# Optimization experiments

Measured on AMD Instinct MI355X. Metric: run time of the kernel, lower is better.

The kernel has to match this reference:

```python
import jax, jax.numpy as jnp
import numpy as np

BETA = 0.25  # commitment-loss weight


def setup_inputs() -> dict:
    key = jax.random.key(0)
    k1, k2 = jax.random.split(key)
    # x: [B, H, W, D] so that x.reshape(-1, D) groups per-pixel latent vectors
    x = jax.random.normal(k1, (32, 64, 64, 64), dtype=jnp.float32)
    # codebook: [D, K] as in the torch module (embedding_dim, num_embeddings)
    embedding = jax.random.normal(k2, (64, 1024), dtype=jnp.float32)
    return {"x": x, "embedding": embedding}


def reference(x, embedding):
    D, K = embedding.shape
    flat = x.reshape(-1, D)  # [N, D]
    # pairwise squared distances: ||z||^2 + ||e||^2 - 2 z.e  -> [N, K]
    distances = (
        jnp.sum(flat * flat, axis=1, keepdims=True)
        + jnp.sum(embedding * embedding, axis=0)
        - 2.0 * (flat @ embedding)
    )
    encoding_indices = jnp.argmin(distances, axis=1)  # [N]
    encodings = jax.nn.one_hot(encoding_indices, K, dtype=x.dtype)  # [N, K]
    # gather codewords (same math as encodings @ embedding.T, but O(N*D))
    quantized = jnp.take(embedding, encoding_indices, axis=1).T.reshape(x.shape)
    e_latent_loss = jnp.mean((jax.lax.stop_gradient(quantized) - x) ** 2)
    loss = BETA * e_latent_loss
    # straight-through estimator
    quantized_st = x + jax.lax.stop_gradient(quantized - x)
    avg_probs = jnp.mean(encodings, axis=0)
    perplexity = jnp.exp(-jnp.sum(avg_probs * jnp.log(avg_probs + 1e-10)))
    return quantized_st, loss, perplexity, encodings, encoding_indices
```

## Files before the change

### kernel.cpp

```cpp
#include <hip/hip_runtime.h>
#include <hip/hip_fp16.h>
#include <math.h>

#define NPIX    131072
#define DDIM    64
#define KCODE   1024
#define BETA    0.25f
#define EPS2    4e-3f
#define FIXCAP  2048
#define TAILROW 130944

#define Q_OFF    0
#define LOSS_OFF 8388608
#define PERP_OFF 8388609
#define ENC_OFF  8388610
#define IDX_OFF  142606338

#define TAIL_F     134086656
#define EHS_F      (TAIL_F + 2)
#define ELS_F      (TAIL_F + 32770)
#define FIXLIST_I  (TAIL_F + 65540)
#define FIXDELTA_F (TAIL_F + 69638)
#define FIXCOUNT_I (TAIL_F + 71688)


typedef _Float16 half8 __attribute__((ext_vector_type(8)));
typedef float    f32x4 __attribute__((ext_vector_type(4)));
typedef __attribute__((address_space(3))) void       lds_void_t;
typedef __attribute__((address_space(1))) const void g_void_t;

__global__ void vq_prep(const float* __restrict__ emb, float* __restrict__ embT,
                        _Float16* __restrict__ ehs, _Float16* __restrict__ els,
                        float* __restrict__ norms) {
    int b = blockIdx.x;
    if (b < 256) {
        int i = b * 256 + threadIdx.x;
        int d = i >> 10;
        int k = i & 1023;
        float v = emb[i];
        embT[k * DDIM + d] = v;
        _Float16 h = (_Float16)v;
        _Float16 l = (_Float16)(v - (float)h);
        int panel = k >> 7, codeP = k & 127;
        int sw = (d >> 3) ^ (k & 7);
        int fi = panel * 8192 + codeP * 64 + sw * 8 + (d & 7);
        ehs[fi] = h;
        els[fi] = l;
    } else {
        int k = (b - 256) * 256 + threadIdx.x;
        float s = 0.f;
        #pragma unroll 8
        for (int d = 0; d < DDIM; ++d) {
            float v = emb[d * KCODE + k];
            s = fmaf(v, v, s);
        }
        norms[k] = s;
    }
}

__global__ __launch_bounds__(256) void vq_argmin_fused(
        const float* __restrict__ x, const _Float16* __restrict__ ehs,
        const _Float16* __restrict__ els, const float* __restrict__ norms,
        const float* __restrict__ embT, float* __restrict__ idxf,
        float* __restrict__ q, float* __restrict__ enc,
        int* __restrict__ hist, float* __restrict__ lossp,
        int* __restrict__ fixlist, int* __restrict__ fixcount) {
    __shared__ __align__(16) char lds_raw[36864];
    half8* EH8   = (half8*)lds_raw;
    half8* EL8   = (half8*)(lds_raw + 16384);
    float* NRMa  = (float*)(lds_raw + 32768);

    const int tid   = threadIdx.x;
    const int blkid = blockIdx.x;
    const int wave  = tid >> 6;
    const int lane  = tid & 63;
    const int lx = lane & 15;
    const int lk = lane >> 4;
    const int pixbase = blkid * 128 + wave * 32;

    #pragma unroll
    for (int i = 0; i < 4; ++i) NRMa[tid + i * 256] = norms[tid + i * 256];

    half8 ah[2][2], al[2][2];
    float xp0 = 0.f, xp1 = 0.f;
    #pragma unroll
    for (int mt = 0; mt < 2; ++mt) {
        const float* xr = x + (size_t)(pixbase + mt * 16 + lx) * DDIM + lk * 8;
        float xps = 0.f;
        #pragma unroll
        for (int kh = 0; kh < 2; ++kh) {
            float4 v0 = *(const float4*)(xr + kh * 32);
            float4 v1 = *(const float4*)(xr + kh * 32 + 4);
            xps = fmaf(v0.x, v0.x, xps); xps = fmaf(v0.y, v0.y, xps);
            xps = fmaf(v0.z, v0.z, xps); xps = fmaf(v0.w, v0.w, xps);
            xps = fmaf(v1.x, v1.x, xps); xps = fmaf(v1.y, v1.y, xps);
            xps = fmaf(v1.z, v1.z, xps); xps = fmaf(v1.w, v1.w, xps);
            half8 hh, ll;
            float vv;
            vv = v0.x; hh[0] = (_Float16)vv; ll[0] = (_Float16)(vv - (float)hh[0]);
            vv = v0.y; hh[1] = (_Float16)vv; ll[1] = (_Float16)(vv - (float)hh[1]);
            vv = v0.z; hh[2] = (_Float16)vv; ll[2] = (_Float16)(vv - (float)hh[2]);
            vv = v0.w; hh[3] = (_Float16)vv; ll[3] = (_Float16)(vv - (float)hh[3]);
            vv = v1.x; hh[4] = (_Float16)vv; ll[4] = (_Float16)(vv - (float)hh[4]);
            vv = v1.y; hh[5] = (_Float16)vv; ll[5] = (_Float16)(vv - (float)hh[5]);
            vv = v1.z; hh[6] = (_Float16)vv; ll[6] = (_Float16)(vv - (float)hh[6]);
            vv = v1.w; hh[7] = (_Float16)vv; ll[7] = (_Float16)(vv - (float)hh[7]);
            ah[mt][kh] = hh;
            al[mt][kh] = ll;
        }
        if (mt == 0) xp0 = xps; else xp1 = xps;
    }
    float xn0 = xp0 + __shfl_xor(xp0, 16); xn0 += __shfl_xor(xn0, 32);
    float xn1 = xp1 + __shfl_xor(xp1, 16); xn1 += __shfl_xor(xn1, 32);

    float b1[2][4], b2[2][4];
    int   i1[2][4];
    #pragma unroll
    for (int mt = 0; mt < 2; ++mt)
        #pragma unroll
        for (int r = 0; r < 4; ++r) { b1[mt][r] = 3.4e38f; b2[mt][r] = 3.4e38f; i1[mt][r] = 0; }

    float* encB = enc + (size_t)blkid * 131072;
    f32x4* zb = (f32x4*)(encB + 2);

    __syncthreads();

    #pragma unroll 1
    for (int t = 0; t < 8; ++t) {
        __builtin_amdgcn_sched_barrier(0);
        __builtin_amdgcn_s_barrier();
        __builtin_amdgcn_sched_barrier(0);
        {
            const char* gH = (const char*)ehs + (t << 14) + (tid << 4);
            const char* gL = (const char*)els + (t << 14) + (tid << 4);
            char* lH = &lds_raw[wave << 10];
            char* lL = &lds_raw[16384 + (wave << 10)];
            #pragma unroll
            for (int i = 0; i < 4; ++i) {
                __builtin_amdgcn_global_load_lds((g_void_t*)(gH + (i << 12)),
                                                 (lds_void_t*)(lH + (i << 12)), 16, 0, 0);
                __builtin_amdgcn_global_load_lds((g_void_t*)(gL + (i << 12)),
                                                 (lds_void_t*)(lL + (i << 12)), 16, 0, 0);
            }
        }
        __builtin_amdgcn_sched_barrier(0);
        if (blkid != 1023) {
            f32x4 z = {0.f, 0.f, 0.f, 0.f};
            #pragma unroll
            for (int it = 0; it < 16; ++it) {
                int fi = t * 4096 + it * 256 + tid;
                if (fi < 32767) zb[fi] = z;
            }
            asm volatile("s_waitcnt vmcnt(16)" ::: "memory");
        } else {
            asm volatile("s_waitcnt vmcnt(0)" ::: "memory");
        }
        __builtin_amdgcn_sched_barrier(0);
        __builtin_amdgcn_s_barrier();
        __builtin_amdgcn_sched_barrier(0);

        const int kbase = t * 128;
        #pragma unroll 1
        for (int c = 0; c < 8; ++c) {
            int code = c * 16 + lx;
            const half8* bhp = EH8 + code * 8;
            const half8* blp = EL8 + code * 8;
            int sw0 = lk ^ (code & 7);
            int sw1 = (lk + 4) ^ (code & 7);
            half8 bh0 = bhp[sw0], bh1 = bhp[sw1];
            half8 bl0 = blp[sw0], bl1 = blp[sw1];

            f32x4 acc0 = {0.f, 0.f, 0.f, 0.f};
            f32x4 acc1 = {0.f, 0.f, 0.f, 0.f};
            acc0 = __builtin_amdgcn_mfma_f32_16x16x32_f16(ah[0][0], bh0, acc0, 0, 0, 0);
            acc1 = __builtin_amdgcn_mfma_f32_16x16x32_f16(ah[1][0], bh0, acc1, 0, 0, 0);
            acc0 = __builtin_amdgcn_mfma_f32_16x16x32_f16(ah[0][1], bh1, acc0, 0, 0, 0);
            acc1 = __builtin_amdgcn_mfma_f32_16x16x32_f16(ah[1][1], bh1, acc1, 0, 0, 0);
            acc0 = __builtin_amdgcn_mfma_f32_16x16x32_f16(ah[0][0], bl0, acc0, 0, 0, 0);
            acc1 = __builtin_amdgcn_mfma_f32_16x16x32_f16(ah[1][0], bl0, acc1, 0, 0, 0);
            acc0 = __builtin_amdgcn_mfma_f32_16x16x32_f16(ah[0][1], bl1, acc0, 0, 0, 0);
            acc1 = __builtin_amdgcn_mfma_f32_16x16x32_f16(ah[1][1], bl1, acc1, 0, 0, 0);
            acc0 = __builtin_amdgcn_mfma_f32_16x16x32_f16(al[0][0], bh0, acc0, 0, 0, 0);
            acc1 = __builtin_amdgcn_mfma_f32_16x16x32_f16(al[1][0], bh0, acc1, 0, 0, 0);
            acc0 = __builtin_amdgcn_mfma_f32_16x16x32_f16(al[0][1], bh1, acc0, 0, 0, 0);
            acc1 = __builtin_amdgcn_mfma_f32_16x16x32_f16(al[1][1], bh1, acc1, 0, 0, 0);

            float nrm = NRMa[kbase + c * 16 + lx];
            int codeg = kbase + c * 16 + lx;
            #pragma unroll
            for (int r = 0; r < 4; ++r) {
                float d0 = fmaf(-2.0f, acc0[r], nrm);
                bool lt0 = d0 < b1[0][r];
                b2[0][r] = fminf(b2[0][r], fmaxf(b1[0][r], d0));
                b1[0][r] = fminf(b1[0][r], d0);
                i1[0][r] = lt0 ? codeg : i1[0][r];
                float d1 = fmaf(-2.0f, acc1[r], nrm);
                bool lt1 = d1 < b1[1][r];
                b2[1][r] = fminf(b2[1][r], fmaxf(b1[1][r], d1));
                b1[1][r] = fminf(b1[1][r], d1);
                i1[1][r] = lt1 ? codeg : i1[1][r];
            }
        }
        __builtin_amdgcn_sched_barrier(0);
    }

    if (blkid != 1023 && tid == 0) {
        encB[0] = 0.f; encB[1] = 0.f;
        encB[131070] = 0.f; encB[131071] = 0.f;
    }
    asm volatile("s_waitcnt vmcnt(0)" ::: "memory");
    __syncthreads();

    float* S  = (float*)(lds_raw + wave * 6528);
    float* SB1 = S, *SI = S + 544, *SB2 = S + 1088;
    int* idx_lds = (int*)(lds_raw + 26112);
    #pragma unroll
    for (int mt = 0; mt < 2; ++mt)
        #pragma unroll
        for (int r = 0; r < 4; ++r) {
            int p = mt * 16 + lk * 4 + r;
            SB1[p * 17 + lx] = b1[mt][r];
            SI [p * 17 + lx] = (float)i1[mt][r];
            SB2[p * 17 + lx] = b2[mt][r];
        }
    __syncthreads();

    float xf0 = __shfl(xn0, lane & 15);
    float xf1 = __shfl(xn1, lane & 15);
    float xf  = (lane >> 4) ? xf1 : xf0;

    float gb1 = 3.4e38f, gb2 = 3.4e38f;
    int gi1 = 0;
    if (lane < 32) {
        gi1 = KCODE;
        #pragma unroll
        for (int j = 0; j < 16; ++j) {
            float cb1 = SB1[lane * 17 + j];
            int   ci1 = (int)SI[lane * 17 + j];
            float cb2 = SB2[lane * 17 + j];
            if (cb1 < gb1 || (cb1 == gb1 && ci1 < gi1)) {
                gb2 = fminf(gb1, cb2); gb1 = cb1; gi1 = ci1;
            } else {
                gb2 = fminf(gb2, cb1);
            }
        }
        int pixel = pixbase + lane;
        idxf[pixel] = (float)gi1;
        idx_lds[wave * 32 + lane] = gi1;
        atomicAdd(&hist[gi1], 1);
        if (blkid != 1023) enc[(size_t)pixel * 1024 + gi1] = 1.f;
        if (gb2 - gb1 < EPS2) {
            int slot = atomicAdd(fixcount, 1);
            if (slot < FIXCAP) {
                fixlist[2 * slot]     = pixel;
                fixlist[2 * slot + 1] = __float_as_int(gb1);
            }
        }
    }

    float sq = (lane < 32) ? (gb1 + xf) : 0.f;
    #pragma unroll
    for (int m = 1; m < 64; m <<= 1) sq += __shfl_xor(sq, m);
    if (lane == 0) lossp[blkid * 4 + wave] = sq;

    __syncthreads();
    const f32x4* eT4 = (const f32x4*)embT;
    f32x4* q4 = (f32x4*)q;
    #pragma unroll
    for (int it = 0; it < 8; ++it) {
        int i = it * 256 + tid;
        int r = i >> 4, j = i & 15;
        int idx = idx_lds[r];
        q4[((size_t)blkid * 128 + r) * 16 + j] = eT4[idx * 16 + j];
    }
}

__global__ __launch_bounds__(64) void vq_fixup(
        const float* __restrict__ x, const float* __restrict__ embT,
        const float* __restrict__ norms, const int* __restrict__ fixlist,
        const int* __restrict__ fixcount, float* __restrict__ idxf,
        float* __restrict__ q, float* __restrict__ enc,
        int* __restrict__ hist, float* __restrict__ fixdelta) {
    int cnt = *fixcount;
    if (cnt > FIXCAP) cnt = FIXCAP;
    int b = blockIdx.x;
    if (b >= cnt) return;
    int pixel = fixlist[2 * b];
    float b1old = __int_as_float(fixlist[2 * b + 1]);
    int lane = threadIdx.x;

    float xr[64];
    const float4* x4 = (const float4*)(x + (size_t)pixel * DDIM);
    #pragma unroll
    for (int j = 0; j < 16; ++j) {
        float4 v = x4[j];
        xr[j * 4] = v.x; xr[j * 4 + 1] = v.y; xr[j * 4 + 2] = v.z; xr[j * 4 + 3] = v.w;
    }
    float bd = 3.4e38f;
    int bi = 0;
    #pragma unroll 1
    for (int c = 0; c < 16; ++c) {
        int k = lane * 16 + c;
        const float4* e4 = (const float4*)(embT + (size_t)k * DDIM);
        float a0 = 0.f, a1 = 0.f, a2 = 0.f, a3 = 0.f;
        #pragma unroll
        for (int j = 0; j < 16; ++j) {
            float4 ev = e4[j];
            a0 = fmaf(xr[j * 4],     ev.x, a0);
            a1 = fmaf(xr[j * 4 + 1], ev.y, a1);
            a2 = fmaf(xr[j * 4 + 2], ev.z, a2);
            a3 = fmaf(xr[j * 4 + 3], ev.w, a3);
        }
        float dd = fmaf(-2.0f, (a0 + a1) + (a2 + a3), norms[k]);
        if (dd < bd) { bd = dd; bi = k; }
    }
    #pragma unroll
    for (int m = 1; m < 64; m <<= 1) {
        float od = __shfl_xor(bd, m, 64);
        int   oi = __shfl_xor(bi, m, 64);
        if (od < bd || (od == bd && oi < bi)) { bd = od; bi = oi; }
    }
    q[(size_t)pixel * DDIM + lane] = embT[(size_t)bi * DDIM + lane];
    if (lane == 0) {
        int old = (int)idxf[pixel];
        idxf[pixel] = (float)bi;
        fixdelta[b] = bd - b1old;
        if (bi != old) {
            atomicAdd(&hist[old], -1);
            atomicAdd(&hist[bi], 1);
            if (pixel < TAILROW) {
                enc[(size_t)pixel * 1024 + old] = 0.f;
                enc[(size_t)pixel * 1024 + bi]  = 1.f;
            }
        }
    }
}

__global__ void vq_final(const float* __restrict__ lossp, const int* __restrict__ hist,
                         const float* __restrict__ fixdelta,
                         const int* __restrict__ fixcount,
                         float* __restrict__ out_loss, float* __restrict__ out_perp) {
    __shared__ double red[256];
    int tid = threadIdx.x;
    double s = 0.0;
    for (int i = tid; i < 4096; i += 256) s += (double)lossp[i];
    red[tid] = s;
    __syncthreads();
    for (int st = 128; st > 0; st >>= 1) {
        if (tid < st) red[tid] += red[tid + st];
        __syncthreads();
    }
    if (tid == 0) {
        int cnt = *fixcount;
        if (cnt > FIXCAP) cnt = FIXCAP;
        double d = red[0];
        for (int i = 0; i < cnt; ++i) d += (double)fixdelta[i];
        *out_loss = (float)((double)BETA * d / (double)((size_t)NPIX * DDIM));
    }
    __syncthreads();

    double e = 0.0;
    for (int i = tid; i < KCODE; i += 256) {
        float p = (float)hist[i] / (float)NPIX;
        e += (double)(p * logf(p + 1e-10f));
    }
    red[tid] = e;
    __syncthreads();
    for (int st = 128; st > 0; st >>= 1) {
        if (tid < st) red[tid] += red[tid + st];
        __syncthreads();
    }
    if (tid == 0) *out_perp = expf((float)(-red[0]));
}

__global__ void vq_tail(const float* __restrict__ idxf, float* __restrict__ enc) {
    int r = blockIdx.x;
    int pixel = TAILROW + r;
    int idx = (int)idxf[pixel];
    size_t base = (size_t)pixel * 1024;
    int t = threadIdx.x;
    if (t < 255) {
        int k = 4 * t + 2;
        f32x4 v;
        v.x = (k     == idx) ? 1.f : 0.f;
        v.y = (k + 1 == idx) ? 1.f : 0.f;
        v.z = (k + 2 == idx) ? 1.f : 0.f;
        v.w = (k + 3 == idx) ? 1.f : 0.f;
        *(f32x4*)(enc + base + k) = v;
    } else {
        enc[base]        = (idx == 0)    ? 1.f : 0.f;
        enc[base + 1]    = (idx == 1)    ? 1.f : 0.f;
        enc[base + 1022] = (idx == 1022) ? 1.f : 0.f;
        enc[base + 1023] = (idx == 1023) ? 1.f : 0.f;
    }
}

extern "C" void kernel_launch(void* const* d_in, const int* in_sizes, int n_in,
                              void* d_out, int out_size, void* d_ws, size_t ws_size,
                              hipStream_t stream) {
    const float* x   = (const float*)d_in[0];
    const float* emb = (const float*)d_in[1];
    float* out = (float*)d_out;

    char* ws = (char*)d_ws;
    float* lossp = (float*)ws;
    int*   hist  = (int*)(ws + 32768);
    float* norms = (float*)(ws + 36864);
    float* embT  = (float*)(ws + 40960);

    float* q      = out + Q_OFF;
    float* o_loss = out + LOSS_OFF;
    float* o_perp = out + PERP_OFF;
    float* enc    = out + ENC_OFF;
    float* idxf   = out + IDX_OFF;

    _Float16* ehs   = (_Float16*)(enc + EHS_F);
    _Float16* els   = (_Float16*)(enc + ELS_F);
    int* fixlist    = (int*)(enc + FIXLIST_I);
    float* fixdelta = (float*)(enc + FIXDELTA_F);
    int* fixcount   = (int*)(enc + FIXCOUNT_I);

    (void)hipMemsetAsync(ws + 32768, 0, 4096, stream);
    (void)hipMemsetAsync((void*)fixcount, 0, 4, stream);

    vq_prep<<<260, 256, 0, stream>>>(emb, embT, ehs, els, norms);
    vq_argmin_fused<<<1024, 256, 0, stream>>>(x, ehs, els, norms, embT, idxf, q,
                                              enc, hist, lossp, fixlist, fixcount);
    vq_fixup<<<FIXCAP, 64, 0, stream>>>(x, embT, norms, fixlist, fixcount,
                                        idxf, q, enc, hist, fixdelta);
    vq_final<<<1, 256, 0, stream>>>(lossp, hist, fixdelta, fixcount, o_loss, o_perp);
    vq_tail<<<128, 256, 0, stream>>>(idxf, enc);
}
```

Baseline: 206.5 us.

## Split encodings zeroing into dedicated blocks and shrink codebook panels

The fused kernel now launches twice as many blocks: odd blocks only stream zeros across the whole one-hot encodings buffer, while even blocks do the fp16-split MFMA argmin. The compute blocks stage 64-code panels instead of 128, which roughly halves LDS use and may raise occupancy. They also reduce candidates with cross-lane shuffles rather than an LDS transpose. The one-hot writes move into a separate poke kernel that must run after zeroing, adding a launch and a reread of the indices in exchange for taking store traffic off the compute waves.

Result: slower. 244.3 us (+18.3%).

```diff
diff --git a/kernel.cpp b/kernel.cpp
--- a/kernel.cpp
+++ b/kernel.cpp
@@ -1,5 +1,4 @@
 #include <hip/hip_runtime.h>
-#include <hip/hip_fp16.h>
 #include <math.h>
 
 #define NPIX    131072
@@ -41,9 +40,9 @@
         embT[k * DDIM + d] = v;
         _Float16 h = (_Float16)v;
         _Float16 l = (_Float16)(v - (float)h);
-        int panel = k >> 7, codeP = k & 127;
+        int panel = k >> 6, codeP = k & 63;
         int sw = (d >> 3) ^ (k & 7);
-        int fi = panel * 8192 + codeP * 64 + sw * 8 + (d & 7);
+        int fi = panel * 4096 + codeP * 64 + sw * 8 + (d & 7);
         ehs[fi] = h;
         els[fi] = l;
     } else {
@@ -58,28 +57,42 @@
     }
 }
 
-__global__ __launch_bounds__(256) void vq_argmin_fused(
+__global__ __launch_bounds__(256) void vq_fused(
         const float* __restrict__ x, const _Float16* __restrict__ ehs,
         const _Float16* __restrict__ els, const float* __restrict__ norms,
         const float* __restrict__ embT, float* __restrict__ idxf,
         float* __restrict__ q, float* __restrict__ enc,
         int* __restrict__ hist, float* __restrict__ lossp,
         int* __restrict__ fixlist, int* __restrict__ fixcount) {
-    __shared__ __align__(16) char lds_raw[36864];
+    __shared__ __align__(16) char lds_raw[17152];
+
+    const int tid  = threadIdx.x;
+    const int role = blockIdx.x & 1;
+    const int rid  = blockIdx.x >> 1;
+
+    if (role == 1) {
+        const long long NSEG = 33521663LL;
+        f32x4* basep = (f32x4*)(enc + 2);
+        f32x4 z = {0.f, 0.f, 0.f, 0.f};
+        long long s = (long long)rid * 256 + tid;
+        for (; s < NSEG; s += 262144LL) basep[s] = z;
+        if (rid == 0 && tid == 0) {
+            enc[0] = 0.f; enc[1] = 0.f;
+            enc[TAIL_F - 2] = 0.f; enc[TAIL_F - 1] = 0.f;
+        }
+        return;
+    }
+
     half8* EH8   = (half8*)lds_raw;
-    half8* EL8   = (half8*)(lds_raw + 16384);
-    float* NRMa  = (float*)(lds_raw + 32768);
-
-    const int tid   = threadIdx.x;
-    const int blkid = blockIdx.x;
-    const int wave  = tid >> 6;
-    const int lane  = tid & 63;
+    half8* EL8   = (half8*)(lds_raw + 8192);
+    float* NRM   = (float*)(lds_raw + 16384);
+    int* idx_lds = (int*)(lds_raw + 16640);
+
+    const int wave = tid >> 6;
+    const int lane = tid & 63;
     const int lx = lane & 15;
     const int lk = lane >> 4;
-    const int pixbase = blkid * 128 + wave * 32;
-
-    #pragma unroll
-    for (int i = 0; i < 4; ++i) NRMa[tid + i * 256] = norms[tid + i * 256];
+    const int pixbase = rid * 128 + wave * 32;
 
     half8 ah[2][2], al[2][2];
     float xp0 = 0.f, xp1 = 0.f;
@@ -120,48 +133,28 @@
         #pragma unroll
         for (int r = 0; r < 4; ++r) { b1[mt][r] = 3.4e38f; b2[mt][r] = 3.4e38f; i1[mt][r] = 0; }
 
-    float* encB = enc + (size_t)blkid * 131072;
-    f32x4* zb = (f32x4*)(encB + 2);
-
-    __syncthreads();
-
     #pragma unroll 1
-    for (int t = 0; t < 8; ++t) {
-        __builtin_amdgcn_sched_barrier(0);
-        __builtin_amdgcn_s_barrier();
-        __builtin_amdgcn_sched_barrier(0);
+    for (int t = 0; t < 16; ++t) {
+        __syncthreads();
         {
-            const char* gH = (const char*)ehs + (t << 14) + (tid << 4);
-            const char* gL = (const char*)els + (t << 14) + (tid << 4);
+            const char* gH = (const char*)ehs + (t << 13) + (tid << 4);
+            const char* gL = (const char*)els + (t << 13) + (tid << 4);
             char* lH = &lds_raw[wave << 10];
-            char* lL = &lds_raw[16384 + (wave << 10)];
+            char* lL = &lds_raw[8192 + (wave << 10)];
             #pragma unroll
-            for (int i = 0; i < 4; ++i) {
+            for (int i = 0; i < 2; ++i) {
                 __builtin_amdgcn_global_load_lds((g_void_t*)(gH + (i << 12)),
                                                  (lds_void_t*)(lH + (i << 12)), 16, 0, 0);
                 __builtin_amdgcn_global_load_lds((g_void_t*)(gL + (i << 12)),
                                                  (lds_void_t*)(lL + (i << 12)), 16, 0, 0);
             }
-        }
-        __builtin_amdgcn_sched_barrier(0);
-        if (blkid != 1023) {
-            f32x4 z = {0.f, 0.f, 0.f, 0.f};
-            #pragma unroll
-            for (int it = 0; it < 16; ++it) {
-                int fi = t * 4096 + it * 256 + tid;
-                if (fi < 32767) zb[fi] = z;
-            }
-            asm volatile("s_waitcnt vmcnt(16)" ::: "memory");
-        } else {
-            asm volatile("s_waitcnt vmcnt(0)" ::: "memory");
-        }
-        __builtin_amdgcn_sched_barrier(0);
-        __builtin_amdgcn_s_barrier();
-        __builtin_amdgcn_sched_barrier(0);
-
-        const int kbase = t * 128;
+            if (tid < 64) NRM[tid] = norms[t * 64 + tid];
+        }
+        __syncthreads();
+
+        const int kbase = t * 64;
         #pragma unroll 1
-        for (int c = 0; c < 8; ++c) {
+        for (int c = 0; c < 4; ++c) {
             int code = c * 16 + lx;
             const half8* bhp = EH8 + code * 8;
             const half8* blp = EL8 + code * 8;
@@ -185,7 +178,7 @@
             acc0 = __builtin_amdgcn_mfma_f32_16x16x32_f16(al[0][1], bh1, acc0, 0, 0, 0);
             acc1 = __builtin_amdgcn_mfma_f32_16x16x32_f16(al[1][1], bh1, acc1, 0, 0, 0);
 
-            float nrm = NRMa[kbase + c * 16 + lx];
+            float nrm = NRM[c * 16 + lx];
             int codeg = kbase + c * 16 + lx;
             #pragma unroll
             for (int r = 0; r < 4; ++r) {
@@ -201,67 +194,64 @@
                 i1[1][r] = lt1 ? codeg : i1[1][r];
             }
         }
-        __builtin_amdgcn_sched_barrier(0);
-    }
-
-    if (blkid != 1023 && tid == 0) {
-        encB[0] = 0.f; encB[1] = 0.f;
-        encB[131070] = 0.f; encB[131071] = 0.f;
-    }
-    asm volatile("s_waitcnt vmcnt(0)" ::: "memory");
-    __syncthreads();
-
-    float* S  = (float*)(lds_raw + wave * 6528);
-    float* SB1 = S, *SI = S + 544, *SB2 = S + 1088;
-    int* idx_lds = (int*)(lds_raw + 26112);
+    }
+
     #pragma unroll
     for (int mt = 0; mt < 2; ++mt)
         #pragma unroll
         for (int r = 0; r < 4; ++r) {
-            int p = mt * 16 + lk * 4 + r;
-            SB1[p * 17 + lx] = b1[mt][r];
-            SI [p * 17 + lx] = (float)i1[mt][r];
-            SB2[p * 17 + lx] = b2[mt][r];
-        }
-    __syncthreads();
-
-    float xf0 = __shfl(xn0, lane & 15);
-    float xf1 = __shfl(xn1, lane & 15);
-    float xf  = (lane >> 4) ? xf1 : xf0;
-
-    float gb1 = 3.4e38f, gb2 = 3.4e38f;
-    int gi1 = 0;
-    if (lane < 32) {
-        gi1 = KCODE;
-        #pragma unroll
-        for (int j = 0; j < 16; ++j) {
-            float cb1 = SB1[lane * 17 + j];
-            int   ci1 = (int)SI[lane * 17 + j];
-            float cb2 = SB2[lane * 17 + j];
-            if (cb1 < gb1 || (cb1 == gb1 && ci1 < gi1)) {
-                gb2 = fminf(gb1, cb2); gb1 = cb1; gi1 = ci1;
-            } else {
-                gb2 = fminf(gb2, cb1);
+            float a1 = b1[mt][r], a2 = b2[mt][r];
+            int   ai = i1[mt][r];
+            #pragma unroll
+            for (int m = 1; m < 16; m <<= 1) {
+                float c1 = __shfl_xor(a1, m, 64);
+                float c2 = __shfl_xor(a2, m, 64);
+                int   ci = __shfl_xor(ai, m, 64);
+                if (c1 < a1 || (c1 == a1 && ci < ai)) {
+                    a2 = fminf(a1, c2); a1 = c1; ai = ci;
+                } else {
+                    a2 = fminf(a2, c1);
+                }
             }
-        }
-        int pixel = pixbase + lane;
-        idxf[pixel] = (float)gi1;
-        idx_lds[wave * 32 + lane] = gi1;
-        atomicAdd(&hist[gi1], 1);
-        if (blkid != 1023) enc[(size_t)pixel * 1024 + gi1] = 1.f;
-        if (gb2 - gb1 < EPS2) {
-            int slot = atomicAdd(fixcount, 1);
-            if (slot < FIXCAP) {
-                fixlist[2 * slot]     = pixel;
-                fixlist[2 * slot + 1] = __float_as_int(gb1);
+            b1[mt][r] = a1; b2[mt][r] = a2; i1[mt][r] = ai;
+        }
+
+    float xfa[2][4];
+    #pragma unroll
+    for (int mt = 0; mt < 2; ++mt)
+        #pragma unroll
+        for (int r = 0; r < 4; ++r)
+            xfa[mt][r] = __shfl(mt == 0 ? xn0 : xn1, lk * 4 + r, 64);
+
+    if (lx == 0) {
+        #pragma unroll
+        for (int mt = 0; mt < 2; ++mt)
+            #pragma unroll
+            for (int r = 0; r < 4; ++r) {
+                int p = mt * 16 + lk * 4 + r;
+                int pixel = pixbase + p;
+                idxf[pixel] = (float)i1[mt][r];
+                idx_lds[wave * 32 + p] = i1[mt][r];
+                atomicAdd(&hist[i1[mt][r]], 1);
+                if (b2[mt][r] - b1[mt][r] < EPS2) {
+                    int slot = atomicAdd(fixcount, 1);
+                    if (slot < FIXCAP) {
+                        fixlist[2 * slot]     = pixel;
+                        fixlist[2 * slot + 1] = __float_as_int(b1[mt][r]);
+                    }
+                }
             }
-        }
-    }
-
-    float sq = (lane < 32) ? (gb1 + xf) : 0.f;
-    #pragma unroll
-    for (int m = 1; m < 64; m <<= 1) sq += __shfl_xor(sq, m);
-    if (lane == 0) lossp[blkid * 4 + wave] = sq;
+    }
+
+    float s8 = 0.f;
+    #pragma unroll
+    for (int mt = 0; mt < 2; ++mt)
+        #pragma unroll
+        for (int r = 0; r < 4; ++r) s8 += b1[mt][r] + xfa[mt][r];
+    float sqv = (lx == 0) ? s8 : 0.f;
+    #pragma unroll
+    for (int m = 1; m < 64; m <<= 1) sqv += __shfl_xor(sqv, m, 64);
+    if (lane == 0) lossp[rid * 4 + wave] = sqv;
 
     __syncthreads();
     const f32x4* eT4 = (const f32x4*)embT;
@@ -271,7 +261,15 @@
         int i = it * 256 + tid;
         int r = i >> 4, j = i & 15;
         int idx = idx_lds[r];
-        q4[((size_t)blkid * 128 + r) * 16 + j] = eT4[idx * 16 + j];
+        q4[((size_t)rid * 128 + r) * 16 + j] = eT4[idx * 16 + j];
+    }
+}
+
+__global__ void vq_poke(const float* __restrict__ idxf, float* __restrict__ enc) {
+    int n = blockIdx.x * 256 + threadIdx.x;
+    if (n < TAILROW) {
+        int idx = (int)idxf[n];
+        enc[(size_t)n * 1024 + idx] = 1.f;
     }
 }
 
@@ -424,8 +422,9 @@
     (void)hipMemsetAsync((void*)fixcount, 0, 4, stream);
 
     vq_prep<<<260, 256, 0, stream>>>(emb, embT, ehs, els, norms);
-    vq_argmin_fused<<<1024, 256, 0, stream>>>(x, ehs, els, norms, embT, idxf, q,
-                                              enc, hist, lossp, fixlist, fixcount);
+    vq_fused<<<2048, 256, 0, stream>>>(x, ehs, els, norms, embT, idxf, q,
+                                       enc, hist, lossp, fixlist, fixcount);
+    vq_poke<<<512, 256, 0, stream>>>(idxf, enc);
     vq_fixup<<<FIXCAP, 64, 0, stream>>>(x, embT, norms, fixlist, fixcount,
                                         idxf, q, enc, hist, fixdelta);
     vq_final<<<1, 256, 0, stream>>>(lossp, hist, fixdelta, fixcount, o_loss, o_perp);
```

## Move one-hot zero fill into separate kernel and tighten fixup threshold

Applied to the files above, without the earlier changes.

Stops the argmin kernel from zero-filling the large one-hot encodings buffer inside its codebook loop and gives that work to a standalone fill kernel launched first. The point is to simplify the main loop's barriers and free it from interleaved stores. The cost is that the zero fill no longer overlaps with MFMA compute and now runs serially before it. It also shrinks the near-tie epsilon used to flag pixels for exact fixup, which cuts fixup work but could miss close ties.

Result: slower. 315.4 us (+52.7%).

```diff
diff --git a/kernel.cpp b/kernel.cpp
--- a/kernel.cpp
+++ b/kernel.cpp
@@ -1,12 +1,11 @@
 #include <hip/hip_runtime.h>
-#include <hip/hip_fp16.h>
 #include <math.h>
 
 #define NPIX    131072
 #define DDIM    64
 #define KCODE   1024
 #define BETA    0.25f
-#define EPS2    4e-3f
+#define EPS2    1e-3f
 #define FIXCAP  2048
 #define TAILROW 130944
 
@@ -28,6 +27,18 @@
 typedef float    f32x4 __attribute__((ext_vector_type(4)));
 typedef __attribute__((address_space(3))) void       lds_void_t;
 typedef __attribute__((address_space(1))) const void g_void_t;
+
+__global__ __launch_bounds__(256) void vq_fill0(float* __restrict__ enc) {
+    const long long NSEG = 33521663LL;
+    f32x4* basep = (f32x4*)(enc + 2);
+    f32x4 z = {0.f, 0.f, 0.f, 0.f};
+    long long s = (long long)blockIdx.x * 256 + threadIdx.x;
+    for (; s < NSEG; s += 524288LL) basep[s] = z;
+    if (blockIdx.x == 0 && threadIdx.x == 0) {
+        enc[0] = 0.f; enc[1] = 0.f;
+        enc[TAIL_F - 2] = 0.f; enc[TAIL_F - 1] = 0.f;
+    }
+}
 
 __global__ void vq_prep(const float* __restrict__ emb, float* __restrict__ embT,
                         _Float16* __restrict__ ehs, _Float16* __restrict__ els,
@@ -120,16 +131,9 @@
         #pragma unroll
         for (int r = 0; r < 4; ++r) { b1[mt][r] = 3.4e38f; b2[mt][r] = 3.4e38f; i1[mt][r] = 0; }
 
-    float* encB = enc + (size_t)blkid * 131072;
-    f32x4* zb = (f32x4*)(encB + 2);
-
-    __syncthreads();
-
     #pragma unroll 1
     for (int t = 0; t < 8; ++t) {
-        __builtin_amdgcn_sched_barrier(0);
-        __builtin_amdgcn_s_barrier();
-        __builtin_amdgcn_sched_barrier(0);
+        __syncthreads();
         {
             const char* gH = (const char*)ehs + (t << 14) + (tid << 4);
             const char* gL = (const char*)els + (t << 14) + (tid << 4);
@@ -143,21 +147,7 @@
                                                  (lds_void_t*)(lL + (i << 12)), 16, 0, 0);
             }
         }
-        __builtin_amdgcn_sched_barrier(0);
-        if (blkid != 1023) {
-            f32x4 z = {0.f, 0.f, 0.f, 0.f};
-            #pragma unroll
-            for (int it = 0; it < 16; ++it) {
-                int fi = t * 4096 + it * 256 + tid;
-                if (fi < 32767) zb[fi] = z;
-            }
-            asm volatile("s_waitcnt vmcnt(16)" ::: "memory");
-        } else {
-            asm volatile("s_waitcnt vmcnt(0)" ::: "memory");
-        }
-        __builtin_amdgcn_sched_barrier(0);
-        __builtin_amdgcn_s_barrier();
-        __builtin_amdgcn_sched_barrier(0);
+        __syncthreads();
 
         const int kbase = t * 128;
         #pragma unroll 1
@@ -201,16 +191,9 @@
                 i1[1][r] = lt1 ? codeg : i1[1][r];
             }
         }
-        __builtin_amdgcn_sched_barrier(0);
-    }
-
-    if (blkid != 1023 && tid == 0) {
-        encB[0] = 0.f; encB[1] = 0.f;
-        encB[131070] = 0.f; encB[131071] = 0.f;
-    }
-    asm volatile("s_waitcnt vmcnt(0)" ::: "memory");
-    __syncthreads();
-
+    }
+
+    __syncthreads();
     float* S  = (float*)(lds_raw + wave * 6528);
     float* SB1 = S, *SI = S + 544, *SB2 = S + 1088;
     int* idx_lds = (int*)(lds_raw + 26112);
@@ -423,6 +406,7 @@
     (void)hipMemsetAsync(ws + 32768, 0, 4096, stream);
     (void)hipMemsetAsync((void*)fixcount, 0, 4, stream);
 
+    vq_fill0<<<2048, 256, 0, stream>>>(enc);
     vq_prep<<<260, 256, 0, stream>>>(emb, embT, ehs, els, norms);
     vq_argmin_fused<<<1024, 256, 0, stream>>>(x, ehs, els, norms, embT, idxf, q,
                                               enc, hist, lossp, fixlist, fixcount);
```
